# Optimization experiments

Hardware: AMD Instinct MI355X
Metric: run time of the kernel (lower is better)

## Reference

```python
import jax, jax.numpy as jnp
import numpy as np

EMB_DIM = 1024
HEAD_NUM = 16
HEAD_DIM = EMB_DIM // HEAD_NUM
B, S = 2, 2048


def setup_inputs() -> dict:
    key = jax.random.key(0)
    k_x, k_wqkv, k_bqkv, k_wo, k_bo = jax.random.split(key, 5)
    x = jax.random.normal(k_x, (B, S, EMB_DIM), dtype=jnp.float32)
    # nn.Linear default init scale ~ 1/sqrt(fan_in); exact distribution irrelevant for a reference
    lim = 1.0 / np.sqrt(EMB_DIM)
    W_qkv = jax.random.uniform(k_wqkv, (EMB_DIM, 3 * EMB_DIM), jnp.float32, -lim, lim)
    b_qkv = jax.random.uniform(k_bqkv, (3 * EMB_DIM,), jnp.float32, -lim, lim)
    W_o = jax.random.uniform(k_wo, (EMB_DIM, EMB_DIM), jnp.float32, -lim, lim)
    b_o = jax.random.uniform(k_bo, (EMB_DIM,), jnp.float32, -lim, lim)
    mask = jnp.tril(jnp.ones((S, S), dtype=bool))  # causal mask as in casual_mask(seq_len)
    return {"x": x, "W_qkv": W_qkv, "b_qkv": b_qkv, "W_o": W_o, "b_o": b_o, "mask": mask}


def reference(x, W_qkv, b_qkv, W_o, b_o, mask):
    b, s, e = x.shape
    qkv = x @ W_qkv + b_qkv                      # [b, s, 3e]
    q, k, v = qkv[..., :e], qkv[..., e:2 * e], qkv[..., 2 * e:]
    # [b, s, h, d] -> [b, h, s, d]
    q = q.reshape(b, s, HEAD_NUM, HEAD_DIM).transpose(0, 2, 1, 3)
    k = k.reshape(b, s, HEAD_NUM, HEAD_DIM).transpose(0, 2, 1, 3)
    v = v.reshape(b, s, HEAD_NUM, HEAD_DIM).transpose(0, 2, 1, 3)
    scores = jnp.einsum("bhqd,bhkd->bhqk", q, k) / jnp.sqrt(jnp.float32(HEAD_DIM))
    scores = jnp.where(mask, scores, -jnp.inf)   # masked_fill(~mask, -inf)
    probs = jax.nn.softmax(scores, axis=-1)      # dropout is identity in eval mode
    out = jnp.einsum("bhqk,bhkd->bhqd", probs, v)
    out = out.transpose(0, 2, 1, 3).reshape(b, s, e)
    return out @ W_o + b_o
```

## Files before the change

### kernel.cpp

```cpp
#include <hip/hip_runtime.h>


typedef __attribute__((ext_vector_type(8))) short short8;
typedef __attribute__((ext_vector_type(4))) short short4v;
typedef __attribute__((ext_vector_type(4))) float floatx4;

#define NB 2
#define SEQ 2048
#define EMB 1024
#define NH 16
#define HD 64
#define M_ROWS (NB * SEQ)
#define N_QKV (3 * EMB)
#define SLOT_B 33792
#define SLOTS_PER_BH 12

#define GLL(g, l) __builtin_amdgcn_global_load_lds( \
    (const __attribute__((address_space(1))) void*)(g), \
    (__attribute__((address_space(3))) void*)(l), 16, 0, 0)

#if defined(__HIP_DEVICE_COMPILE__)
#define MFMA16K16(A, B, C) __builtin_amdgcn_mfma_f32_16x16x16bf16_1k(A, B, C, 0, 0, 0)
#else
#define MFMA16K16(A, B, C) (C)
#endif

static __device__ __forceinline__ unsigned short f2bf(float f) {
    union { float f; unsigned int u; } v; v.f = f;
    unsigned int r = v.u + 0x7FFFu + ((v.u >> 16) & 1u);
    return (unsigned short)(r >> 16);
}
static __device__ __forceinline__ float bf2f(unsigned short h) {
    union { unsigned int u; float f; } v; v.u = ((unsigned int)h) << 16;
    return v.f;
}

static __device__ __forceinline__ unsigned int cvt_pk_bf16(float lo, float hi) {
#if defined(__HIP_DEVICE_COMPILE__)
    unsigned int r;
    asm("v_cvt_pk_bf16_f32 %0, %1, %2" : "=v"(r) : "v"(lo), "v"(hi));
    return r;
#else
    (void)lo; (void)hi; return 0u;
#endif
}
static __device__ __forceinline__ short4v pack4bf(float a, float b, float c, float d) {
    union { unsigned int u[2]; short4v s; } pu;
    pu.u[0] = cvt_pk_bf16(a, b);
    pu.u[1] = cvt_pk_bf16(c, d);
    return pu.s;
}

__constant__ unsigned char FQT[20] = {
    1,3,3,5,5,5,7,7,7,7, 4,4,6,6,6,6, 2,2,4, 0 };
__constant__ unsigned char FCI[20] = {
    0,0,1,0,1,2,0,1,2,3, 1,2,0,1,2,3, 0,1,0, 0 };

static __device__ __forceinline__ int slot_off(int qt3, int ci) {
    int so = (qt3 < 4) ? (qt3 - 2)
           : (qt3 < 6 ? 2 + (qt3 - 4) * 2 : 6 + (qt3 - 6) * 3);
    return so + (ci - 1);
}

__global__ void prep(const float* __restrict__ x,
                     const float* __restrict__ Wqkv, const float* __restrict__ Wo,
                     unsigned short* __restrict__ x_bf,
                     unsigned short* __restrict__ wqkvT, unsigned short* __restrict__ woT) {
    __shared__ unsigned short tile[32][33];
    int z = blockIdx.z;
    int tx = threadIdx.x, ty = threadIdx.y;
    if (z == 2) {
        int id = ((int)blockIdx.y * 96 + (int)blockIdx.x) * 256 + ty * 32 + tx;
        const int n4 = M_ROWS * EMB / 4;
        for (int i = id; i < n4; i += 96 * 32 * 256) {
            float4 v = ((const float4*)x)[i];
            unsigned long long p = (unsigned long long)f2bf(v.x)
                | ((unsigned long long)f2bf(v.y) << 16)
                | ((unsigned long long)f2bf(v.z) << 32)
                | ((unsigned long long)f2bf(v.w) << 48);
            ((unsigned long long*)x_bf)[i] = p;
        }
        return;
    }
    int C = z ? EMB : N_QKV;
    if ((int)blockIdx.x * 32 >= C) return;
    const float* in = z ? Wo : Wqkv;
    unsigned short* out = z ? woT : wqkvT;
    const int R = EMB;
    int c0 = blockIdx.x * 32, r0 = blockIdx.y * 32;
    #pragma unroll
    for (int j = 0; j < 4; ++j)
        tile[ty + j * 8][tx] = f2bf(in[(size_t)(r0 + ty + j * 8) * C + c0 + tx]);
    __syncthreads();
    #pragma unroll
    for (int j = 0; j < 4; ++j)
        out[(size_t)(c0 + ty + j * 8) * R + r0 + tx] = tile[tx][ty + j * 8];
}

#define CTS 130

__global__ __launch_bounds__(256) void qkv_gemm(
    const unsigned short* __restrict__ A,
    const unsigned short* __restrict__ Bt,
    const float* __restrict__ bias,
    unsigned short* __restrict__ qb, unsigned short* __restrict__ kb,
    unsigned short* __restrict__ vb)
{
    const int K = EMB;
    __shared__ __align__(16) unsigned short smem[128 * CTS];

    int t = threadIdx.x;
    int m0 = blockIdx.y * 128;
    int n0 = blockIdx.x * 128;
    int w = t >> 6, lane = t & 63, quad = lane >> 4, lcol = lane & 15;
    int wr = w >> 1, wc = w & 1;

    floatx4 zero = {0.f, 0.f, 0.f, 0.f};
    floatx4 acc[4][4];
    #pragma unroll
    for (int i = 0; i < 4; ++i)
        #pragma unroll
        for (int j = 0; j < 4; ++j) acc[i][j] = zero;

    const unsigned short* a0 = A  + (size_t)(m0 + (t >> 2)) * K + ((t & 3) << 3);
    const unsigned short* b0 = Bt + (size_t)(n0 + (t >> 2)) * K + ((t & 3) << 3);
    unsigned short* la = &smem[t << 3];

    GLL(a0, la);
    GLL(a0 + 64 * K, la + 2048);
    GLL(b0, la + 4096);
    GLL(b0 + 64 * K, la + 6144);

    for (int k0 = 0; k0 < K; k0 += 32) {
        int cur = (k0 >> 5) & 1, nxt = cur ^ 1;
        __syncthreads();
        if (k0 + 32 < K) {
            GLL(a0 + k0 + 32, la + nxt * 8192);
            GLL(a0 + 64 * K + k0 + 32, la + nxt * 8192 + 2048);
            GLL(b0 + k0 + 32, la + nxt * 8192 + 4096);
            GLL(b0 + 64 * K + k0 + 32, la + nxt * 8192 + 6144);
        }
        const unsigned short* As = &smem[cur * 8192];
        const unsigned short* Bs = As + 4096;
        short8 af[4], bfm[4];
        #pragma unroll
        for (int i = 0; i < 4; ++i)
            af[i] = *(const short8*)(&As[(wr * 64 + i * 16 + lcol) * 32 + quad * 8]);
        #pragma unroll
        for (int j = 0; j < 4; ++j)
            bfm[j] = *(const short8*)(&Bs[(wc * 64 + j * 16 + lcol) * 32 + quad * 8]);
        #pragma unroll
        for (int i = 0; i < 4; ++i)
            #pragma unroll
            for (int j = 0; j < 4; ++j)
                acc[i][j] = __builtin_amdgcn_mfma_f32_16x16x32_bf16(af[i], bfm[j], acc[i][j], 0, 0, 0);
    }

    bool isV = (n0 >= 2 * EMB);
    __syncthreads();
    #pragma unroll
    for (int i = 0; i < 4; ++i) {
        int row0 = wr * 64 + i * 16 + quad * 4;
        #pragma unroll
        for (int j = 0; j < 4; ++j) {
            int col = wc * 64 + j * 16 + lcol;
            float bv = bias[n0 + col];
            #pragma unroll
            for (int r = 0; r < 4; ++r) {
                unsigned short hv = f2bf(acc[i][j][r] + bv);
                if (isV) smem[col * CTS + row0 + r] = hv;
                else     smem[(row0 + r) * CTS + col] = hv;
            }
        }
    }
    __syncthreads();

    int b = m0 >> 11, s0 = m0 & 2047;
    int hbase = (n0 & 1023) >> 6;
    if (!isV) {
        unsigned short* dst = (n0 >= EMB) ? kb : qb;
        #pragma unroll
        for (int it = 0; it < 8; ++it) {
            int job = it * 32 + (t >> 3);
            int tok = job & 127, hh = job >> 7;
            int chunk = t & 7;
            short8 vv = *(const short8*)(&smem[tok * CTS + hh * 64 + chunk * 8]);
            size_t g = ((size_t)((b * NH + hbase + hh) * SEQ + s0 + tok)) * HD + chunk * 8;
            *(short8*)(&dst[g]) = vv;
        }
    } else {
        #pragma unroll
        for (int it = 0; it < 8; ++it) {
            int job = it * 32 + (t >> 3);
            int f = job & 127, half = job >> 7;
            int chunk = (t & 7) + half * 8;
            short8 vv = *(const short8*)(&smem[f * CTS + chunk * 8]);
            int h = hbase + (f >> 6), d = f & 63;
            size_t g = ((size_t)((b * NH + h) * HD + d)) * SEQ + s0 + chunk * 8;
            *(short8*)(&vb[g]) = vv;
        }
    }
}

__global__ __launch_bounds__(512) void attn_fused(
    const unsigned short* __restrict__ Q,
    const unsigned short* __restrict__ Kk,
    const unsigned short* __restrict__ Vt,
    unsigned short* __restrict__ Out,
    unsigned char* __restrict__ Part,
    float* __restrict__ Laux)
{
    __shared__ __align__(16) unsigned short Ks[3][64 * 64];
    __shared__ __align__(16) unsigned short Vs[3][64 * 64];

    int fid = (int)blockIdx.y * 20 + (int)blockIdx.x;
    int bh  = (fid & 7) * 4 + ((fid >> 3) & 3);
    int qq  = fid >> 5;
    int qt3 = FQT[qq];
    int ci  = FCI[qq];
    int nc  = (qt3 + 2) >> 1;
    int nt  = 4 * (qt3 + 1);
    int t0  = (nt * ci) / nc, t1 = (nt * (ci + 1)) / nc;
    int q0  = qt3 * 256;

    int t = threadIdx.x;
    int w = t >> 6, lane = t & 63, quad = lane >> 4, lcol = lane & 15;
    const size_t hoff = (size_t)bh * SEQ * HD;
    const float SC = 0.18033688011112043f;

    short8 aq[2][2];
    #pragma unroll
    for (int g = 0; g < 2; ++g) {
        const unsigned short* qp = Q + hoff
            + (size_t)(q0 + g * 128 + 16 * w + lcol) * HD + quad * 8;
        aq[g][0] = *(const short8*)qp;
        aq[g][1] = *(const short8*)(qp + 32);
    }
    asm volatile("s_waitcnt vmcnt(0)" ::: "memory");

    int srow = t >> 3;
    int ss   = (t & 7) ^ (srow & 7);
    const unsigned short* kgl = Kk + hoff + (size_t)srow * HD + ss * 8;
    const unsigned short* vgl = Vt + hoff + (size_t)srow * SEQ + ss * 8;
    unsigned short* kld = &Ks[0][t * 8];
    unsigned short* vld = &Vs[0][t * 8];

#define STAGE(kt_, buf_) do { \
        size_t kk_ = (size_t)(kt_) * 64; \
        GLL(kgl + kk_ * HD, kld + (buf_) * 4096); \
        GLL(vgl + kk_,      vld + (buf_) * 4096); \
    } while (0)

    floatx4 zero = {0.f, 0.f, 0.f, 0.f};
    floatx4 O[2][4];
    floatx4 lacc[2];
    #pragma unroll
    for (int g = 0; g < 2; ++g) {
        lacc[g] = zero;
        #pragma unroll
        for (int td = 0; td < 4; ++td) O[g][td] = zero;
    }

    short4v ones4;
    #pragma unroll
    for (int jj = 0; jj < 4; ++jj) ones4[jj] = (short)0x3F80;

    STAGE(t0, t0 % 3);
    if (t0 + 1 < t1) STAGE(t0 + 1, (t0 + 1) % 3);

    int sx0 = (quad ^ (lcol & 7)) << 3;
    int sx1 = sx0 ^ 32;

    for (int kt = t0; kt < t1; ++kt) {
        if (kt + 1 < t1) asm volatile("s_waitcnt vmcnt(2)" ::: "memory");
        else             asm volatile("s_waitcnt vmcnt(0)" ::: "memory");
        __builtin_amdgcn_s_barrier();
        __builtin_amdgcn_sched_barrier(0);

        int b3 = kt % 3;
        const unsigned short* ksr = &Ks[b3][0];
        const unsigned short* vsr = &Vs[b3][0];

        short4v pk[2][4];
        bool act[2];
        #pragma unroll
        for (int g = 0; g < 2; ++g) {
            const int gb = q0 + g * 128 + 16 * w;
            act[g] = (kt * 64 <= gb + 15);
            if (act[g]) {
                short8 bk0[4], bk1[4];
                #pragma unroll
                for (int tc = 0; tc < 4; ++tc) {
                    int rb = (tc * 16 + lcol) << 6;
                    bk0[tc] = *(const short8*)(ksr + rb + sx0);
                    bk1[tc] = *(const short8*)(ksr + rb + sx1);
                }
                floatx4 sacc[4];
                #pragma unroll
                for (int tc = 0; tc < 4; ++tc) {
                    sacc[tc] = __builtin_amdgcn_mfma_f32_16x16x32_bf16(bk0[tc], aq[g][0], zero, 0, 0, 0);
                    sacc[tc] = __builtin_amdgcn_mfma_f32_16x16x32_bf16(bk1[tc], aq[g][1], sacc[tc], 0, 0, 0);
                }
                if (kt * 64 + 63 > gb) {
                    int qrow = gb + lcol;
                    #pragma unroll
                    for (int tc = 0; tc < 4; ++tc) {
                        float p[4];
                        #pragma unroll
                        for (int r = 0; r < 4; ++r) {
                            float e = __builtin_amdgcn_exp2f(sacc[tc][r] * SC);
                            p[r] = (kt * 64 + tc * 16 + quad * 4 + r > qrow) ? 0.f : e;
                        }
                        pk[g][tc] = pack4bf(p[0], p[1], p[2], p[3]);
                    }
                } else {
                    #pragma unroll
                    for (int tc = 0; tc < 4; ++tc) {
                        pk[g][tc] = pack4bf(
                            __builtin_amdgcn_exp2f(sacc[tc][0] * SC),
                            __builtin_amdgcn_exp2f(sacc[tc][1] * SC),
                            __builtin_amdgcn_exp2f(sacc[tc][2] * SC),
                            __builtin_amdgcn_exp2f(sacc[tc][3] * SC));
                    }
                }
            }
        }

        if (act[0]) {
            #pragma unroll
            for (int td = 0; td < 4; ++td) {
                short4v va[4];
                #pragma unroll
                for (int tc = 0; tc < 4; ++tc) {
                    int seg = ((tc << 1) + (quad >> 1)) ^ (lcol & 7);
                    va[tc] = *(const short4v*)(vsr + ((td * 16 + lcol) << 6) + (seg << 3) + ((quad & 1) << 2));
                }
                #pragma unroll
                for (int tc = 0; tc < 4; ++tc)
                    O[0][td] = MFMA16K16(va[tc], pk[0][tc], O[0][td]);
                if (act[1]) {
                    #pragma unroll
                    for (int tc = 0; tc < 4; ++tc)
                        O[1][td] = MFMA16K16(va[tc], pk[1][tc], O[1][td]);
                }
            }
        } else if (act[1]) {
            #pragma unroll
            for (int td = 0; td < 4; ++td) {
                short4v va[4];
                #pragma unroll
                for (int tc = 0; tc < 4; ++tc) {
                    int seg = ((tc << 1) + (quad >> 1)) ^ (lcol & 7);
                    va[tc] = *(const short4v*)(vsr + ((td * 16 + lcol) << 6) + (seg << 3) + ((quad & 1) << 2));
                }
                #pragma unroll
                for (int tc = 0; tc < 4; ++tc)
                    O[1][td] = MFMA16K16(va[tc], pk[1][tc], O[1][td]);
            }
        }
        #pragma unroll
        for (int g = 0; g < 2; ++g) {
            if (act[g]) {
                #pragma unroll
                for (int tc = 0; tc < 4; ++tc)
                    lacc[g] = MFMA16K16(ones4, pk[g][tc], lacc[g]);
            }
        }

        __builtin_amdgcn_sched_barrier(0);
        if (kt + 2 < t1) STAGE(kt + 2, (kt + 2) % 3);
    }
#undef STAGE

    if (nc == 1) {
        int b = bh >> 4, h = bh & 15;
        #pragma unroll
        for (int g = 0; g < 2; ++g) {
            int qrow = q0 + g * 128 + 16 * w + lcol;
            float inv = 1.0f / lacc[g][0];
            size_t obase = ((size_t)b * SEQ + qrow) * EMB + (size_t)h * HD + quad * 4;
            #pragma unroll
            for (int td = 0; td < 4; ++td) {
                short4v ov;
                #pragma unroll
                for (int r = 0; r < 4; ++r) ov[r] = (short)f2bf(O[g][td][r] * inv);
                *(short4v*)(&Out[obase + td * 16]) = ov;
            }
        }
    } else if (ci == 0) {
        int b = bh >> 4, h = bh & 15;
        float* lrow = Laux + ((size_t)bh * 6 + (qt3 - 2)) * 256;
        #pragma unroll
        for (int g = 0; g < 2; ++g) {
            int ql = g * 128 + 16 * w + lcol;
            int qrow = q0 + ql;
            size_t obase = ((size_t)b * SEQ + qrow) * EMB + (size_t)h * HD + quad * 4;
            #pragma unroll
            for (int td = 0; td < 4; ++td) {
                short4v ov;
                #pragma unroll
                for (int r = 0; r < 4; ++r) ov[r] = (short)f2bf(O[g][td][r]);
                *(short4v*)(&Out[obase + td * 16]) = ov;
            }
            if (quad == 0) lrow[ql] = lacc[g][0];
        }
    } else {
        unsigned char* sp = Part
            + (size_t)(bh * SLOTS_PER_BH + slot_off(qt3, ci)) * SLOT_B;
        unsigned short* sO = (unsigned short*)sp;
        float* sL = (float*)(sp + 32768);
        #pragma unroll
        for (int g = 0; g < 2; ++g) {
            int ql = g * 128 + 16 * w + lcol;
            #pragma unroll
            for (int td = 0; td < 4; ++td) {
                short4v ov;
                #pragma unroll
                for (int r = 0; r < 4; ++r) ov[r] = (short)f2bf(O[g][td][r]);
                *(short4v*)(&sO[ql * 64 + td * 16 + quad * 4]) = ov;
            }
            if (quad == 0) sL[ql] = lacc[g][0];
        }
    }
}

__global__ __launch_bounds__(256) void attn_combine(
    const unsigned char* __restrict__ Part, const float* __restrict__ Laux,
    unsigned short* __restrict__ Out)
{
    int qt3 = 2 + (int)blockIdx.x;
    int bh = blockIdx.y;
    int nc = (qt3 + 2) >> 1;
    const unsigned char* base = Part
        + (size_t)(bh * SLOTS_PER_BH + slot_off(qt3, 1)) * SLOT_B;
    const float* lrow = Laux + ((size_t)bh * 6 + (qt3 - 2)) * 256;
    int b = bh >> 4, h = bh & 15;
    size_t obase = ((size_t)b * SEQ + qt3 * 256) * EMB + (size_t)h * HD;
    int t = threadIdx.x;
    #pragma unroll
    for (int it = 0; it < 8; ++it) {
        int job = it * 256 + t;
        int row = job >> 3, c8 = (job & 7) * 8;
        unsigned short* op = &Out[obase + (size_t)row * EMB + c8];
        float acc8[8];
        short8 v0 = *(const short8*)op;
        #pragma unroll
        for (int e = 0; e < 8; ++e) acc8[e] = bf2f((unsigned short)v0[e]);
        float lsum = lrow[row];
        for (int k = 1; k < nc; ++k) {
            const unsigned char* sp = base + (size_t)(k - 1) * SLOT_B;
            const unsigned short* sO = (const unsigned short*)sp;
            const float* sL = (const float*)(sp + 32768);
            short8 vv = *(const short8*)(&sO[row * 64 + c8]);
            #pragma unroll
            for (int e = 0; e < 8; ++e) acc8[e] += bf2f((unsigned short)vv[e]);
            lsum += sL[row];
        }
        float inv = 1.0f / lsum;
        short8 ov;
        #pragma unroll
        for (int e = 0; e < 8; ++e) ov[e] = (short)f2bf(acc8[e] * inv);
        *(short8*)op = ov;
    }
}

__global__ __launch_bounds__(256) void oproj_gemm(
    const unsigned short* __restrict__ A,
    const unsigned short* __restrict__ Bt,
    const float* __restrict__ bias,
    float* __restrict__ Cout)
{
    const int K = EMB;
    __shared__ __align__(16) unsigned short smem[3 * 8192];
    int t = threadIdx.x;
    int m0 = blockIdx.y * 128;
    int n0 = blockIdx.x * 128;
    int w = t >> 6, lane = t & 63, quad = lane >> 4, lcol = lane & 15;
    int wr = w >> 1, wc = w & 1;

    floatx4 zero = {0.f, 0.f, 0.f, 0.f};
    floatx4 acc[4][4];
    #pragma unroll
    for (int i = 0; i < 4; ++i)
        #pragma unroll
        for (int j = 0; j < 4; ++j) acc[i][j] = zero;

    const unsigned short* a0 = A  + (size_t)(m0 + (t >> 2)) * K + ((t & 3) << 3);
    const unsigned short* b0 = Bt + (size_t)(n0 + (t >> 2)) * K + ((t & 3) << 3);
    unsigned short* la = &smem[t << 3];

#define OSTAGE(k0_, b_) do { \
        GLL(a0 + (k0_), la + (b_) * 8192); \
        GLL(a0 + 64 * K + (k0_), la + (b_) * 8192 + 2048); \
        GLL(b0 + (k0_), la + (b_) * 8192 + 4096); \
        GLL(b0 + 64 * K + (k0_), la + (b_) * 8192 + 6144); \
    } while (0)

    OSTAGE(0, 0);
    OSTAGE(32, 1);

    for (int k0 = 0; k0 < K; k0 += 32) {
        int it = k0 >> 5;
        if (k0 + 32 < K) asm volatile("s_waitcnt vmcnt(4)" ::: "memory");
        else             asm volatile("s_waitcnt vmcnt(0)" ::: "memory");
        __builtin_amdgcn_s_barrier();
        __builtin_amdgcn_sched_barrier(0);

        const unsigned short* As = &smem[(it % 3) * 8192];
        const unsigned short* Bs = As + 4096;
        short8 af[4], bfm[4];
        #pragma unroll
        for (int i = 0; i < 4; ++i)
            af[i] = *(const short8*)(&As[(wr * 64 + i * 16 + lcol) * 32 + quad * 8]);
        #pragma unroll
        for (int j = 0; j < 4; ++j)
            bfm[j] = *(const short8*)(&Bs[(wc * 64 + j * 16 + lcol) * 32 + quad * 8]);
        #pragma unroll
        for (int i = 0; i < 4; ++i)
            #pragma unroll
            for (int j = 0; j < 4; ++j)
                acc[i][j] = __builtin_amdgcn_mfma_f32_16x16x32_bf16(af[i], bfm[j], acc[i][j], 0, 0, 0);

        __builtin_amdgcn_sched_barrier(0);
        if (k0 + 64 < K) OSTAGE(k0 + 64, (it + 2) % 3);
    }
#undef OSTAGE

    #pragma unroll
    for (int i = 0; i < 4; ++i) {
        int m = m0 + wr * 64 + i * 16 + quad * 4;
        #pragma unroll
        for (int j = 0; j < 4; ++j) {
            int n = n0 + wc * 64 + j * 16 + lcol;
            float bv = bias[n];
            #pragma unroll
            for (int r = 0; r < 4; ++r)
                Cout[(size_t)(m + r) * EMB + n] = acc[i][j][r] + bv;
        }
    }
}

extern "C" void kernel_launch(void* const* d_in, const int* in_sizes, int n_in,
                              void* d_out, int out_size, void* d_ws, size_t ws_size,
                              hipStream_t stream) {
    (void)in_sizes; (void)n_in; (void)out_size; (void)ws_size;
    char* ws = (char*)d_ws;
    const size_t OFF_X     = 0;
    const size_t OFF_WQKVT = OFF_X     + (size_t)M_ROWS * EMB * 2;
    const size_t OFF_WOT   = OFF_WQKVT + (size_t)N_QKV * EMB * 2;
    const size_t OFF_Q     = OFF_WOT   + (size_t)EMB * EMB * 2;
    const size_t OFF_K     = OFF_Q     + (size_t)M_ROWS * EMB * 2;
    const size_t OFF_V     = OFF_K     + (size_t)M_ROWS * EMB * 2;
    const size_t OFF_ATTN  = OFF_V     + (size_t)M_ROWS * EMB * 2;
    const size_t OFF_PART  = OFF_X;
    const size_t OFF_LAUX  = OFF_PART + (size_t)32 * SLOTS_PER_BH * SLOT_B;

    const float* x    = (const float*)d_in[0];
    const float* Wqkv = (const float*)d_in[1];
    const float* bqkv = (const float*)d_in[2];
    const float* Wo   = (const float*)d_in[3];
    const float* bo   = (const float*)d_in[4];

    unsigned short* x_bf  = (unsigned short*)(ws + OFF_X);
    unsigned short* wqkvT = (unsigned short*)(ws + OFF_WQKVT);
    unsigned short* woT   = (unsigned short*)(ws + OFF_WOT);
    unsigned short* qb    = (unsigned short*)(ws + OFF_Q);
    unsigned short* kb    = (unsigned short*)(ws + OFF_K);
    unsigned short* vb    = (unsigned short*)(ws + OFF_V);
    unsigned short* attn  = (unsigned short*)(ws + OFF_ATTN);
    unsigned char*  part  = (unsigned char*)(ws + OFF_PART);
    float*          laux  = (float*)(ws + OFF_LAUX);

    prep<<<dim3(96, 32, 3), dim3(32, 8), 0, stream>>>(x, Wqkv, Wo, x_bf, wqkvT, woT);

    qkv_gemm<<<dim3(N_QKV / 128, M_ROWS / 128), 256, 0, stream>>>(x_bf, wqkvT, bqkv, qb, kb, vb);
    attn_fused<<<dim3(20, NB * NH), 512, 0, stream>>>(qb, kb, vb, attn, part, laux);
    attn_combine<<<dim3(6, NB * NH), 256, 0, stream>>>(part, laux, attn);
    oproj_gemm<<<dim3(EMB / 128, M_ROWS / 128), 256, 0, stream>>>(attn, woT, bo, (float*)d_out);
}
```

Baseline: 193.7 us.

## Triple-buffer QKV GEMM LDS loads with explicit vmcnt waits

Moves the QKV projection GEMM from double to triple buffering of its A and B tiles in LDS, prefetching two k-steps ahead with async global-to-LDS loads. It replaces the per-iteration __syncthreads with an explicit s_waitcnt vmcnt plus s_barrier and uses sched barriers to keep the MFMA block separate from the next prefetch. The aim is to hide more global load latency behind the MFMAs. In exchange it uses more shared memory per block, which can lower occupancy, and it relies on hand-counted vmcnt values being correct.

```diff
diff --git a/kernel.cpp b/kernel.cpp
--- a/kernel.cpp
+++ b/kernel.cpp
@@ -107,7 +107,7 @@
     unsigned short* __restrict__ vb)
 {
     const int K = EMB;
-    __shared__ __align__(16) unsigned short smem[128 * CTS];
+    __shared__ __align__(16) unsigned short smem[3 * 8192];
 
     int t = threadIdx.x;
     int m0 = blockIdx.y * 128;
@@ -126,21 +126,24 @@
     const unsigned short* b0 = Bt + (size_t)(n0 + (t >> 2)) * K + ((t & 3) << 3);
     unsigned short* la = &smem[t << 3];
 
-    GLL(a0, la);
-    GLL(a0 + 64 * K, la + 2048);
-    GLL(b0, la + 4096);
-    GLL(b0 + 64 * K, la + 6144);
+#define QSTAGE(k0_, b_) do { \
+        GLL(a0 + (k0_), la + (b_) * 8192); \
+        GLL(a0 + 64 * K + (k0_), la + (b_) * 8192 + 2048); \
+        GLL(b0 + (k0_), la + (b_) * 8192 + 4096); \
+        GLL(b0 + 64 * K + (k0_), la + (b_) * 8192 + 6144); \
+    } while (0)
+
+    QSTAGE(0, 0);
+    QSTAGE(32, 1);
 
     for (int k0 = 0; k0 < K; k0 += 32) {
-        int cur = (k0 >> 5) & 1, nxt = cur ^ 1;
-        __syncthreads();
-        if (k0 + 32 < K) {
-            GLL(a0 + k0 + 32, la + nxt * 8192);
-            GLL(a0 + 64 * K + k0 + 32, la + nxt * 8192 + 2048);
-            GLL(b0 + k0 + 32, la + nxt * 8192 + 4096);
-            GLL(b0 + 64 * K + k0 + 32, la + nxt * 8192 + 6144);
-        }
-        const unsigned short* As = &smem[cur * 8192];
+        int it = k0 >> 5;
+        if (k0 + 32 < K) asm volatile("s_waitcnt vmcnt(4)" ::: "memory");
+        else             asm volatile("s_waitcnt vmcnt(0)" ::: "memory");
+        __builtin_amdgcn_s_barrier();
+        __builtin_amdgcn_sched_barrier(0);
+
+        const unsigned short* As = &smem[(it % 3) * 8192];
         const unsigned short* Bs = As + 4096;
         short8 af[4], bfm[4];
         #pragma unroll
@@ -154,7 +157,11 @@
             #pragma unroll
             for (int j = 0; j < 4; ++j)
                 acc[i][j] = __builtin_amdgcn_mfma_f32_16x16x32_bf16(af[i], bfm[j], acc[i][j], 0, 0, 0);
-    }
+
+        __builtin_amdgcn_sched_barrier(0);
+        if (k0 + 64 < K) QSTAGE(k0 + 64, (it + 2) % 3);
+    }
+#undef QSTAGE
 
     bool isV = (n0 >= 2 * EMB);
     __syncthreads();
```

New measurement: 198.6 us. 1.03x slower.
